# Optimization experiments

Measured on AMD Instinct MI355X. Metric: run time of the kernel, lower is better.

The kernel has to match this reference:

```python
import jax, jax.numpy as jnp
import numpy as np

K = 5
BASE_LAMBDA = 0.05
BASE_DELTA = 0.01
ITERS = 3
STEP = 0.2
FUSION_SCALE = 2.0
EPS = 1e-8


def _param_sets():
    # Deterministic (jitter_strength=0) version of SASConfig._generate_param_sets.
    # View 0 is identity; views 1..K-1 get linearly spaced lambda and coupled delta.
    lmin, lmax = BASE_LAMBDA * 0.5, BASE_LAMBDA * 1.5
    lams, deltas = [], []
    for i in range(K - 1):
        lam = lmin + (lmax - lmin) * i / max(1, K - 2)
        lams.append(lam)
        deltas.append(BASE_DELTA * np.sqrt(lam / (BASE_LAMBDA + 1e-8)))
    return jnp.asarray(lams, jnp.float32), jnp.asarray(deltas, jnp.float32)


def _huber_tv(x, lam, delta):
    # Anisotropic Huber-TV diffusion, skip_clamp=True (artifact denoising path).
    # x: [B,C,H,W]
    xd = x
    for _ in range(ITERS):
        dx = jnp.pad(xd[:, :, :, 1:] - xd[:, :, :, :-1], ((0, 0), (0, 0), (0, 0), (0, 1)))
        dy = jnp.pad(xd[:, :, 1:, :] - xd[:, :, :-1, :], ((0, 0), (0, 0), (0, 1), (0, 0)))
        gx = dx / (delta + jnp.abs(dx))
        gy = dy / (delta + jnp.abs(dy))
        # divergence with replicated first element (div[...,0] = g[...,0])
        div_x = gx - jnp.pad(gx[:, :, :, :-1], ((0, 0), (0, 0), (0, 0), (1, 0)))
        div_y = gy - jnp.pad(gy[:, :, :-1, :], ((0, 0), (0, 0), (1, 0), (0, 0)))
        xd = xd - STEP * (xd - x - lam * (div_x + div_y))
    return xd


def setup_inputs() -> dict:
    key = jax.random.key(0)
    x = jax.random.normal(key, (32, 3, 256, 256), dtype=jnp.float32)
    return {"x": x}


def reference(x):
    B = x.shape[0]
    # torch.median over flattened |artifact| (lower median for even count)
    flat = jnp.abs(x).reshape(B, -1)
    n = flat.shape[1]
    scale = jnp.sort(flat, axis=1)[:, (n - 1) // 2].reshape(B, 1, 1, 1) + 1e-8

    lams, deltas = _param_sets()
    xn = x / scale
    denoised = jax.vmap(lambda l, d: _huber_tv(xn, l, d))(lams, deltas)  # [K-1,B,C,H,W]
    arts = jnp.concatenate([x[None], denoised * scale[None]], axis=0)  # [K,B,C,H,W]

    # Robust MAD-weighted fusion (K=5 is odd, jnp.median == torch.median over dim 0)
    med = jnp.median(arts, axis=0)
    dev = jnp.abs(arts - med[None])
    mad = jnp.median(dev, axis=0)
    mad = jnp.maximum(mad, 0.1 * mad.mean())
    w = jnp.exp(-dev / (FUSION_SCALE * mad[None]))
    fused = (w * arts).sum(axis=0) / (w.sum(axis=0) + EPS)
    return fused
```

## Files before the change

### kernel.cpp

```cpp
#include <hip/hip_runtime.h>
#include <math.h>

typedef unsigned int u32;
typedef unsigned long long u64;

#define NPIX 6291456


__device__ __forceinline__ float med3f(float a, float b, float c) {
    return fmaxf(fminf(a, b), fminf(fmaxf(a, b), c));
}
__device__ __forceinline__ float med5f(float a0, float a1, float a2, float a3, float a4) {
    float mn01 = fminf(a0, a1), mx01 = fmaxf(a0, a1);
    float mn34 = fminf(a3, a4), mx34 = fmaxf(a3, a4);
    return med3f(a2, fmaxf(mn01, mn34), fminf(mx01, mx34));
}
__device__ __forceinline__ u32 packbf(float lo, float hi) {
    u32 a = __float_as_uint(lo), b = __float_as_uint(hi);
    a = (a + 0x7FFFu + ((a >> 16) & 1u)) >> 16;
    b = (b + 0x7FFFu + ((b >> 16) & 1u)) >> 16;
    return a | (b << 16);
}

__device__ __forceinline__ u32 scan1024(u32 v, u32* wtot) {
    int lane = threadIdx.x & 63, wid = threadIdx.x >> 6;
    u32 inc = v;
    #pragma unroll
    for (int off = 1; off < 64; off <<= 1) {
        u32 o = __shfl_up(inc, off);
        if (lane >= off) inc += o;
    }
    __syncthreads();
    if (lane == 63) wtot[wid] = inc;
    __syncthreads();
    for (int w = 0; w < wid; ++w) inc += wtot[w];
    return inc;
}


__global__ __launch_bounds__(1024) void hist_kernel(
        const float* __restrict__ x, u32* __restrict__ hist,
        float* __restrict__ madsum) {
    __shared__ u32 lh[16400];
    int b = blockIdx.x >> 3, s = blockIdx.x & 7, t = threadIdx.x;
    uint4 z = make_uint4(0u, 0u, 0u, 0u);
    #pragma unroll
    for (int j = 0; j < 4; ++j) ((uint4*)lh)[t + j * 1024] = z;
    if (t < 4) ((uint4*)lh)[4096 + t] = z;
    __syncthreads();
    const float4* xb = (const float4*)(x + (size_t)b * 196608 + s * 24576);
    u32 sub = (u32)(t & 3) * 4100u;
    #pragma unroll
    for (int i = 0; i < 6; ++i) {
        float4 v = xb[t + i * 1024];
        atomicAdd(&lh[sub + (__float_as_uint(fabsf(v.x)) >> 19)], 1u);
        atomicAdd(&lh[sub + (__float_as_uint(fabsf(v.y)) >> 19)], 1u);
        atomicAdd(&lh[sub + (__float_as_uint(fabsf(v.z)) >> 19)], 1u);
        atomicAdd(&lh[sub + (__float_as_uint(fabsf(v.w)) >> 19)], 1u);
    }
    __syncthreads();
    u32 a0 = 0, a1 = 0, a2 = 0, a3 = 0;
    #pragma unroll
    for (int sb = 0; sb < 4; ++sb) {
        uint4 hv = *(const uint4*)&lh[sb * 4100u + (u32)t * 4u];
        a0 += hv.x; a1 += hv.y; a2 += hv.z; a3 += hv.w;
    }
    u32* hb = hist + ((size_t)b * 8 + s) * 4096;
    ((uint4*)hb)[t] = make_uint4(a0, a1, a2, a3);
    if (s == 0 && t == 0 && b == 0) *madsum = 0.0f;
}


__global__ __launch_bounds__(1024) void extract_kernel(
        const float* __restrict__ x, const u32* __restrict__ hist,
        u32* __restrict__ members, u32* __restrict__ scount,
        u32* __restrict__ selBin, u32* __restrict__ selKr) {
    __shared__ u32 sbuf[8192];
    __shared__ u32 wtot[16];
    __shared__ u32 sBin, lcnt;
    int b = blockIdx.x >> 3, s = blockIdx.x & 7, t = threadIdx.x, lane = t & 63;
    if (t == 0) lcnt = 0u;
    const u32* hb = hist + (size_t)b * 32768;
    u32 s4[4] = {0u, 0u, 0u, 0u};
    #pragma unroll
    for (int sl = 0; sl < 8; ++sl) {
        uint4 h4 = ((const uint4*)(hb + sl * 4096))[t];
        s4[0] += h4.x; s4[1] += h4.y; s4[2] += h4.z; s4[3] += h4.w;
    }
    u32 sum = s4[0] + s4[1] + s4[2] + s4[3];
    u32 inc = scan1024(sum, wtot);
    u32 exc = inc - sum;
    u32 k = 98303u;
    if (exc <= k && k < inc) {
        u32 kr = k - exc;
        int j = 0;
        while (kr >= s4[j]) { kr -= s4[j]; ++j; }
        sBin = (u32)(t * 4 + j);
        if (s == 0) { selBin[b] = (u32)(t * 4 + j); selKr[b] = kr; }
    }
    __syncthreads();
    u32 bin = sBin;
    const float4* xb = (const float4*)(x + (size_t)b * 196608 + s * 24576);
    #pragma unroll 2
    for (int i = 0; i < 6; ++i) {
        float4 v = xb[t + i * 1024];
        float vv[4] = {v.x, v.y, v.z, v.w};
        #pragma unroll
        for (int e = 0; e < 4; ++e) {
            u32 bits = __float_as_uint(fabsf(vv[e]));
            bool is = (bits >> 19) == bin;
            u64 ball = __ballot(is);
            if (ball) {
                u32 cnt = (u32)__popcll(ball);
                u32 base = 0;
                if (lane == 0) base = atomicAdd(&lcnt, cnt);
                base = __shfl(base, 0);
                if (is) {
                    u32 p = base + (u32)__popcll(ball & ((1ull << lane) - 1ull));
                    if (p < 8192u) sbuf[p] = bits & 0x7FFFFu;
                }
            }
        }
    }
    __syncthreads();
    u32 cnt = lcnt; if (cnt > 8192u) cnt = 8192u;
    u32* mb = members + ((size_t)b * 8 + s) * 8192;
    for (u32 i = (u32)t; i < cnt; i += 1024u) mb[i] = sbuf[i];
    if (t == 0) scount[b * 8 + s] = cnt;
}


__global__ __launch_bounds__(1024) void select_kernel(
        const u32* __restrict__ scount, const u32* __restrict__ members,
        const u32* __restrict__ selBin, const u32* __restrict__ selKr,
        float* __restrict__ scale) {
    __shared__ u32 sbuf[8192];
    __shared__ u32 h[128];
    __shared__ u32 wtot[16];
    __shared__ u32 sPfx, sK;
    int b = blockIdx.x, t = threadIdx.x;
    u32 c[8], off[8], tot = 0u;
    #pragma unroll
    for (int s = 0; s < 8; ++s) {
        c[s] = scount[b * 8 + s];
        off[s] = tot;
        tot += c[s];
    }
    #pragma unroll
    for (int s = 0; s < 8; ++s) {
        const u32* mb = members + ((size_t)b * 8 + s) * 8192;
        for (u32 i = (u32)t; i < c[s]; i += 1024u) {
            u32 p = off[s] + i;
            if (p < 8192u) sbuf[p] = mb[i];
        }
    }
    u32 m = tot; if (m > 8192u) m = 8192u;
    if (t == 0) { sPfx = 0u; sK = selKr[b]; }
    __syncthreads();
    const int shf[3] = {12, 6, 0};
    const int wd[3]  = {7, 6, 6};
    const u32 msk[3] = {127u, 63u, 63u};
    #pragma unroll 1
    for (int rd = 0; rd < 3; ++rd) {
        u32 pfx = sPfx, k2 = sK;
        if (t < 128) h[t] = 0u;
        __syncthreads();
        for (u32 i = (u32)t; i < m; i += 1024u) {
            u32 v = sbuf[i];
            if ((v >> (shf[rd] + wd[rd])) == pfx)
                atomicAdd(&h[(v >> shf[rd]) & msk[rd]], 1u);
        }
        __syncthreads();
        u32 nb = msk[rd] + 1u;
        u32 cc = ((u32)t < nb) ? h[t] : 0u;
        u32 inc2 = scan1024(cc, wtot);
        u32 exc2 = inc2 - cc;
        if ((u32)t < nb && exc2 <= k2 && k2 < inc2) {
            sPfx = (pfx << wd[rd]) | (u32)t;
            sK = k2 - exc2;
        }
        __syncthreads();
    }
    if (t == 0)
        scale[b] = __uint_as_float((selBin[b] << 19) | sPfx) + 1e-8f;
}


__device__ __forceinline__ float dpp_shl1(float v) {
    return __uint_as_float((u32)__builtin_amdgcn_update_dpp(
        0, (int)__float_as_uint(v), 0x130, 0xF, 0xF, true));
}
__device__ __forceinline__ float dpp_shr1(float v) {
    return __uint_as_float((u32)__builtin_amdgcn_update_dpp(
        0, (int)__float_as_uint(v), 0x138, 0xF, 0xF, true));
}
__device__ __forceinline__ float hub(float d, float del) {
    return d * __builtin_amdgcn_rcpf(del + fabsf(d));
}
__device__ __forceinline__ float upd(float b, float xn, float dv, float lam) {
    float t = fmaf(-lam, dv, b - xn);
    return fmaf(-0.2f, t, b);
}

__device__ __forceinline__ float4 stage4(float4 B, float4 C, float4 xn, float4& gyp,
                                         int row, float mR3, float mL0,
                                         float lam, float del) {
    float mr = (row < 255) ? 1.f : 0.f;
    float m0 = (row == 0) ? 0.f : 1.f;
    float gy0 = hub(C.x - B.x, del) * mr;
    float gy1 = hub(C.y - B.y, del) * mr;
    float gy2 = hub(C.z - B.z, del) * mr;
    float gy3 = hub(C.w - B.w, del) * mr;
    float dv0 = gy0 - gyp.x * m0;
    float dv1 = gy1 - gyp.y * m0;
    float dv2 = gy2 - gyp.z * m0;
    float dv3 = gy3 - gyp.w * m0;
    gyp.x = gy0; gyp.y = gy1; gyp.z = gy2; gyp.w = gy3;
    float B0n = dpp_shl1(B.x);
    float g01 = hub(B.y - B.x, del);
    float g12 = hub(B.z - B.y, del);
    float g23 = hub(B.w - B.z, del);
    float g3n = hub(B0n - B.w, del) * mR3;
    float gp  = dpp_shr1(g3n) * mL0;
    float4 o;
    o.x = upd(B.x, xn.x, (g01 - gp)  + dv0, lam);
    o.y = upd(B.y, xn.y, (g12 - g01) + dv1, lam);
    o.z = upd(B.z, xn.z, (g23 - g12) + dv2, lam);
    o.w = upd(B.w, xn.w, (g3n - g23) + dv3, lam);
    return o;
}

__global__ __launch_bounds__(256, 6) void denoise_kernel(
        const float* __restrict__ x, const float* __restrict__ scale,
        u32* __restrict__ arts, float* __restrict__ madsum,
        float4 lam4, float4 del4) {
    __shared__ float sex[2][5][256];
    __shared__ float red[4];
    int t = threadIdx.x, lane = t & 63, wid = t >> 6;
    int img = blockIdx.x >> 3;
    int seg = blockIdx.x & 7;
    float sc = scale[img / 3];
    float lam = ((wid == 0) ? lam4.x : (wid == 1) ? lam4.y : (wid == 2) ? lam4.z : lam4.w) * sc;
    float del = ((wid == 0) ? del4.x : (wid == 1) ? del4.y : (wid == 2) ? del4.z : del4.w) * sc;
    float mR3 = (lane == 63) ? 0.f : 1.f;
    float mL0 = (lane == 0) ? 0.f : 1.f;
    const float4* xp = (const float4*)(x + (size_t)img * 65536) + lane;
    u32* ap = arts + (size_t)wid * (NPIX / 2) + (size_t)img * 32768 + lane * 2;

    float4 z4 = {0.f, 0.f, 0.f, 0.f};
    float4 cur1 = z4, cur2 = z4, gyp1 = z4, gyp2 = z4, gyp3 = z4;
    float4 n0 = z4, n1 = z4, n2 = z4;
    int out_lo = seg * 32, out_hi = out_lo + 31;
    int rs = (out_lo >= 3) ? out_lo - 3 : 0;
    int rend = out_hi + 3;
    float msum = 0.f;

    float4 nl = xp[rs << 6];
    for (int r = rs; r <= rend; ++r) {
        int rn = (r + 1 <= 255) ? r + 1 : 255;
        float4 nxt = xp[rn << 6];
        int r1 = r - 1, r2 = r - 2, r3 = r - 3;
        float4 x1 = stage4(n0,   nl, n0, gyp1, r1, mR3, mL0, lam, del);
        float4 x2 = stage4(cur1, x1, n1, gyp2, r2, mR3, mL0, lam, del);
        float4 x3 = stage4(cur2, x2, n2, gyp3, r3, mR3, mL0, lam, del);
        cur1 = x1; cur2 = x2;
        if (r3 >= out_lo) {
            uint2 pk;
            pk.x = packbf(x3.x, x3.y);
            pk.y = packbf(x3.z, x3.w);
            *(uint2*)(ap + (r3 << 7)) = pk;
            int pb = r3 & 1;
            *(float4*)&sex[pb][wid + 1][lane * 4] = x3;
            if (wid == 0) *(float4*)&sex[pb][0][lane * 4] = n2;
            __syncthreads();
            int c = wid * 64 + lane;
            float a0 = sex[pb][0][c], a1 = sex[pb][1][c], a2 = sex[pb][2][c],
                  a3 = sex[pb][3][c], a4 = sex[pb][4][c];
            float med = med5f(a0, a1, a2, a3, a4);
            msum += med5f(fabsf(a0 - med), fabsf(a1 - med), fabsf(a2 - med),
                          fabsf(a3 - med), fabsf(a4 - med));
        }
        n2 = n1; n1 = n0; n0 = nl;
        nl = nxt;
    }
    #pragma unroll
    for (int off = 32; off > 0; off >>= 1) msum += __shfl_down(msum, off);
    if (lane == 0) red[wid] = msum;
    __syncthreads();
    if (t == 0) atomicAdd(madsum, red[0] + red[1] + red[2] + red[3]);
}


__global__ __launch_bounds__(256) void fuse_kernel(
        const float* __restrict__ x, const u32* __restrict__ artsU,
        const float* __restrict__ madsum, float* __restrict__ out) {
    int t = blockIdx.x * 256 + threadIdx.x;
    float floorv = 0.1f * (*madsum) * (1.0f / 6291456.0f);
    float4 xv = ((const float4*)x)[t];
    uint2 q0 = ((const uint2*)(artsU))[t];
    uint2 q1 = ((const uint2*)(artsU + NPIX / 2))[t];
    uint2 q2 = ((const uint2*)(artsU + NPIX))[t];
    uint2 q3 = ((const uint2*)(artsU + 3 * (NPIX / 2)))[t];
    float4 o;
#define FUSE1(res, A0, U0, U1, U2, U3, SH) { \
        float a0 = A0; \
        float a1 = __uint_as_float(SH(U0)), a2 = __uint_as_float(SH(U1)); \
        float a3 = __uint_as_float(SH(U2)), a4 = __uint_as_float(SH(U3)); \
        float med = med5f(a0, a1, a2, a3, a4); \
        float d0 = fabsf(a0 - med), d1 = fabsf(a1 - med), d2 = fabsf(a2 - med); \
        float d3 = fabsf(a3 - med), d4 = fabsf(a4 - med); \
        float mad = med5f(d0, d1, d2, d3, d4); \
        float mm = fmaxf(mad, floorv); \
        float inv = 0.5f / mm; \
        float w0 = __expf(-d0 * inv), w1 = __expf(-d1 * inv), w2 = __expf(-d2 * inv); \
        float w3 = __expf(-d3 * inv), w4 = __expf(-d4 * inv); \
        float swt = w0 + w1 + w2 + w3 + w4; \
        float sva = fmaf(w0, a0, fmaf(w1, a1, fmaf(w2, a2, fmaf(w3, a3, w4 * a4)))); \
        res = sva / (swt + 1e-8f); \
    }
#define LO16(u) ((u) << 16)
#define HI16(u) ((u) & 0xFFFF0000u)
    FUSE1(o.x, xv.x, q0.x, q1.x, q2.x, q3.x, LO16);
    FUSE1(o.y, xv.y, q0.x, q1.x, q2.x, q3.x, HI16);
    FUSE1(o.z, xv.z, q0.y, q1.y, q2.y, q3.y, LO16);
    FUSE1(o.w, xv.w, q0.y, q1.y, q2.y, q3.y, HI16);
#undef FUSE1
#undef LO16
#undef HI16
    ((float4*)out)[t] = o;
}


extern "C" void kernel_launch(void* const* d_in, const int* in_sizes, int n_in,
                              void* d_out, int out_size, void* d_ws, size_t ws_size,
                              hipStream_t stream) {
    const float* x = (const float*)d_in[0];
    float* out = (float*)d_out;
    char* ws = (char*)d_ws;
    float* scale  = (float*)ws;
    float* madsum = (float*)(ws + 128);
    u32* selBin   = (u32*)(ws + 384);
    u32* selKr    = (u32*)(ws + 512);
    u32* artsU    = (u32*)(ws + 1024);
    u32* hist     = artsU;
    u32* members  = artsU + (size_t)32 * 8 * 4096;
    u32* scount   = members + (size_t)32 * 8 * 8192;

    hist_kernel<<<256, 1024, 0, stream>>>(x, hist, madsum);
    extract_kernel<<<256, 1024, 0, stream>>>(x, hist, members, scount, selBin, selKr);
    select_kernel<<<32, 1024, 0, stream>>>(scount, members, selBin, selKr, scale);

    float lamf[4], delf[4];
    for (int i = 0; i < 4; ++i) {
        double lam = 0.025 + 0.05 * (double)i / 3.0;
        lamf[i] = (float)lam;
        delf[i] = (float)(0.01 * sqrt(lam / (0.05 + 1e-8)));
    }
    float4 lam4 = make_float4(lamf[0], lamf[1], lamf[2], lamf[3]);
    float4 del4 = make_float4(delf[0], delf[1], delf[2], delf[3]);

    denoise_kernel<<<768, 256, 0, stream>>>(x, scale, artsU, madsum, lam4, del4);
    fuse_kernel<<<6144, 256, 0, stream>>>(x, artsU, madsum, out);
}
```

Before: 177.8 us.

## Merge all stages into one cooperative persistent kernel with grid syncs

```diff
diff --git a/kernel.cpp b/kernel.cpp
--- a/kernel.cpp
+++ b/kernel.cpp
@@ -1,10 +1,15 @@
 #include <hip/hip_runtime.h>
+#include <hip/hip_cooperative_groups.h>
 #include <math.h>
+
+namespace cg = cooperative_groups;
 
 typedef unsigned int u32;
 typedef unsigned long long u64;
 
 #define NPIX 6291456
+#define NBLK 768
+#define NTHR 256
 
 
 __device__ __forceinline__ float med3f(float a, float b, float c) {
@@ -22,7 +27,7 @@
     return a | (b << 16);
 }
 
-__device__ __forceinline__ u32 scan1024(u32 v, u32* wtot) {
+__device__ __forceinline__ u32 scan256(u32 v, u32* wtot) {
     int lane = threadIdx.x & 63, wid = threadIdx.x >> 6;
     u32 inc = v;
     #pragma unroll
@@ -38,72 +43,85 @@
 }
 
 
-__global__ __launch_bounds__(1024) void hist_kernel(
-        const float* __restrict__ x, u32* __restrict__ hist,
-        float* __restrict__ madsum) {
-    __shared__ u32 lh[16400];
-    int b = blockIdx.x >> 3, s = blockIdx.x & 7, t = threadIdx.x;
+__device__ void phase_hist(const float* __restrict__ x, u32* ghist,
+                           float* madsum, u32* shraw) {
+    int blk = blockIdx.x, t = threadIdx.x;
+    int b = blk / 24, s = blk % 24;
+    u32* lh = shraw;
     uint4 z = make_uint4(0u, 0u, 0u, 0u);
     #pragma unroll
-    for (int j = 0; j < 4; ++j) ((uint4*)lh)[t + j * 1024] = z;
-    if (t < 4) ((uint4*)lh)[4096 + t] = z;
-    __syncthreads();
-    const float4* xb = (const float4*)(x + (size_t)b * 196608 + s * 24576);
-    u32 sub = (u32)(t & 3) * 4100u;
-    #pragma unroll
-    for (int i = 0; i < 6; ++i) {
-        float4 v = xb[t + i * 1024];
-        atomicAdd(&lh[sub + (__float_as_uint(fabsf(v.x)) >> 19)], 1u);
-        atomicAdd(&lh[sub + (__float_as_uint(fabsf(v.y)) >> 19)], 1u);
-        atomicAdd(&lh[sub + (__float_as_uint(fabsf(v.z)) >> 19)], 1u);
-        atomicAdd(&lh[sub + (__float_as_uint(fabsf(v.w)) >> 19)], 1u);
-    }
-    __syncthreads();
-    u32 a0 = 0, a1 = 0, a2 = 0, a3 = 0;
-    #pragma unroll
-    for (int sb = 0; sb < 4; ++sb) {
-        uint4 hv = *(const uint4*)&lh[sb * 4100u + (u32)t * 4u];
-        a0 += hv.x; a1 += hv.y; a2 += hv.z; a3 += hv.w;
-    }
-    u32* hb = hist + ((size_t)b * 8 + s) * 4096;
-    ((uint4*)hb)[t] = make_uint4(a0, a1, a2, a3);
-    if (s == 0 && t == 0 && b == 0) *madsum = 0.0f;
-}
-
-
-__global__ __launch_bounds__(1024) void extract_kernel(
-        const float* __restrict__ x, const u32* __restrict__ hist,
-        u32* __restrict__ members, u32* __restrict__ scount,
-        u32* __restrict__ selBin, u32* __restrict__ selKr) {
-    __shared__ u32 sbuf[8192];
-    __shared__ u32 wtot[16];
-    __shared__ u32 sBin, lcnt;
-    int b = blockIdx.x >> 3, s = blockIdx.x & 7, t = threadIdx.x, lane = t & 63;
-    if (t == 0) lcnt = 0u;
-    const u32* hb = hist + (size_t)b * 32768;
-    u32 s4[4] = {0u, 0u, 0u, 0u};
-    #pragma unroll
-    for (int sl = 0; sl < 8; ++sl) {
-        uint4 h4 = ((const uint4*)(hb + sl * 4096))[t];
-        s4[0] += h4.x; s4[1] += h4.y; s4[2] += h4.z; s4[3] += h4.w;
-    }
-    u32 sum = s4[0] + s4[1] + s4[2] + s4[3];
-    u32 inc = scan1024(sum, wtot);
+    for (int j = 0; j < 4; ++j) ((uint4*)lh)[t + j * 256] = z;
+    __syncthreads();
+    const float4* xb = (const float4*)(x + (size_t)b * 196608 + s * 8192);
+    #pragma unroll
+    for (int i = 0; i < 8; ++i) {
+        float4 v = xb[t + i * 256];
+        atomicAdd(&lh[__float_as_uint(fabsf(v.x)) >> 19], 1u);
+        atomicAdd(&lh[__float_as_uint(fabsf(v.y)) >> 19], 1u);
+        atomicAdd(&lh[__float_as_uint(fabsf(v.z)) >> 19], 1u);
+        atomicAdd(&lh[__float_as_uint(fabsf(v.w)) >> 19], 1u);
+    }
+    __syncthreads();
+    uint4* ghb = (uint4*)(ghist + (size_t)blk * 4096);
+    #pragma unroll
+    for (int j = 0; j < 4; ++j) ghb[t + j * 256] = ((uint4*)lh)[t + j * 256];
+    if (blk == 0 && t == 0) *madsum = 0.0f;
+}
+
+
+__device__ void phase_binsel(const u32* ghist, u32* selBin, u32* selKr,
+                             u32* shraw) {
+    int blk = blockIdx.x;
+    if (blk >= 32) return;
+    int t = threadIdx.x;
+    u32* wtot = shraw;
+    u32 s16[16];
+    #pragma unroll
+    for (int j = 0; j < 16; ++j) s16[j] = 0u;
+    const u32* hb = ghist + (size_t)blk * 24 * 4096;
+    for (int sl = 0; sl < 24; ++sl) {
+        const uint4* hp = (const uint4*)(hb + sl * 4096);
+        #pragma unroll
+        for (int j = 0; j < 4; ++j) {
+            uint4 h4 = hp[t * 4 + j];
+            s16[4 * j + 0] += h4.x; s16[4 * j + 1] += h4.y;
+            s16[4 * j + 2] += h4.z; s16[4 * j + 3] += h4.w;
+        }
+    }
+    u32 sum = 0;
+    #pragma unroll
+    for (int j = 0; j < 16; ++j) sum += s16[j];
+    u32 inc = scan256(sum, wtot);
     u32 exc = inc - sum;
     u32 k = 98303u;
     if (exc <= k && k < inc) {
-        u32 kr = k - exc;
-        int j = 0;
-        while (kr >= s4[j]) { kr -= s4[j]; ++j; }
-        sBin = (u32)(t * 4 + j);
-        if (s == 0) { selBin[b] = (u32)(t * 4 + j); selKr[b] = kr; }
-    }
-    __syncthreads();
-    u32 bin = sBin;
-    const float4* xb = (const float4*)(x + (size_t)b * 196608 + s * 24576);
+        u32 kr = k - exc, acc = 0u;
+        #pragma unroll
+        for (int j = 0; j < 16; ++j) {
+            u32 nacc = acc + s16[j];
+            if (kr >= acc && kr < nacc) {
+                selBin[blk] = (u32)(t * 16 + j);
+                selKr[blk] = kr - acc;
+            }
+            acc = nacc;
+        }
+    }
+}
+
+
+__device__ void phase_extract(const float* __restrict__ x, const u32* selBin,
+                              u32* members, u32* scount, u32* shraw) {
+    int blk = blockIdx.x, t = threadIdx.x, lane = t & 63;
+    int b = blk / 24, s = blk % 24;
+    u32* sbuf = shraw;
+    u32* lcnt = shraw + 8192;
+    if (t == 0) *lcnt = 0u;
+    u32 bin = selBin[b];
+    __syncthreads();
+    const float4* xb = (const float4*)(x + (size_t)b * 196608 + s * 8192);
     #pragma unroll 2
-    for (int i = 0; i < 6; ++i) {
-        float4 v = xb[t + i * 1024];
+    for (int i = 0; i < 8; ++i) {
+        float4 v = xb[t + i * 256];
         float vv[4] = {v.x, v.y, v.z, v.w};
         #pragma unroll
         for (int e = 0; e < 4; ++e) {
@@ -113,7 +131,7 @@
             if (ball) {
                 u32 cnt = (u32)__popcll(ball);
                 u32 base = 0;
-                if (lane == 0) base = atomicAdd(&lcnt, cnt);
+                if (lane == 0) base = atomicAdd(lcnt, cnt);
                 base = __shfl(base, 0);
                 if (is) {
                     u32 p = base + (u32)__popcll(ball & ((1ull << lane) - 1ull));
@@ -123,49 +141,52 @@
         }
     }
     __syncthreads();
-    u32 cnt = lcnt; if (cnt > 8192u) cnt = 8192u;
-    u32* mb = members + ((size_t)b * 8 + s) * 8192;
-    for (u32 i = (u32)t; i < cnt; i += 1024u) mb[i] = sbuf[i];
-    if (t == 0) scount[b * 8 + s] = cnt;
-}
-
-
-__global__ __launch_bounds__(1024) void select_kernel(
-        const u32* __restrict__ scount, const u32* __restrict__ members,
-        const u32* __restrict__ selBin, const u32* __restrict__ selKr,
-        float* __restrict__ scale) {
-    __shared__ u32 sbuf[8192];
-    __shared__ u32 h[128];
-    __shared__ u32 wtot[16];
-    __shared__ u32 sPfx, sK;
-    int b = blockIdx.x, t = threadIdx.x;
-    u32 c[8], off[8], tot = 0u;
-    #pragma unroll
-    for (int s = 0; s < 8; ++s) {
-        c[s] = scount[b * 8 + s];
-        off[s] = tot;
-        tot += c[s];
-    }
-    #pragma unroll
-    for (int s = 0; s < 8; ++s) {
-        const u32* mb = members + ((size_t)b * 8 + s) * 8192;
-        for (u32 i = (u32)t; i < c[s]; i += 1024u) {
-            u32 p = off[s] + i;
+    u32 cnt = *lcnt; if (cnt > 8192u) cnt = 8192u;
+    u32* mb = members + (size_t)blk * 8192;
+    for (u32 i = (u32)t; i < cnt; i += 256u) mb[i] = sbuf[i];
+    if (t == 0) scount[blk] = cnt;
+}
+
+
+__device__ void phase_select(const u32* scount, const u32* members,
+                             const u32* selBin, const u32* selKr,
+                             float* scale, u32* shraw) {
+    int blk = blockIdx.x;
+    if (blk >= 32) return;
+    int t = threadIdx.x;
+    u32* sbuf = shraw;
+    u32* h    = shraw + 8192;
+    u32* wtot = shraw + 8320;
+    u32* soff = shraw + 8336;
+    u32* sPfx = shraw + 8364;
+    u32* sK   = shraw + 8365;
+    if (t == 0) {
+        u32 acc = 0u;
+        for (int sl = 0; sl < 24; ++sl) { soff[sl] = acc; acc += scount[blk * 24 + sl]; }
+        soff[24] = acc;
+        *sPfx = 0u;
+        *sK = selKr[blk];
+    }
+    __syncthreads();
+    for (int sl = 0; sl < 24; ++sl) {
+        u32 off = soff[sl], c = soff[sl + 1] - off;
+        const u32* mb = members + (size_t)(blk * 24 + sl) * 8192;
+        for (u32 i = (u32)t; i < c; i += 256u) {
+            u32 p = off + i;
             if (p < 8192u) sbuf[p] = mb[i];
         }
     }
-    u32 m = tot; if (m > 8192u) m = 8192u;
-    if (t == 0) { sPfx = 0u; sK = selKr[b]; }
+    u32 m = soff[24]; if (m > 8192u) m = 8192u;
     __syncthreads();
     const int shf[3] = {12, 6, 0};
     const int wd[3]  = {7, 6, 6};
     const u32 msk[3] = {127u, 63u, 63u};
     #pragma unroll 1
     for (int rd = 0; rd < 3; ++rd) {
-        u32 pfx = sPfx, k2 = sK;
+        u32 pfx = *sPfx, k2 = *sK;
         if (t < 128) h[t] = 0u;
         __syncthreads();
-        for (u32 i = (u32)t; i < m; i += 1024u) {
+        for (u32 i = (u32)t; i < m; i += 256u) {
             u32 v = sbuf[i];
             if ((v >> (shf[rd] + wd[rd])) == pfx)
                 atomicAdd(&h[(v >> shf[rd]) & msk[rd]], 1u);
@@ -173,16 +194,16 @@
         __syncthreads();
         u32 nb = msk[rd] + 1u;
         u32 cc = ((u32)t < nb) ? h[t] : 0u;
-        u32 inc2 = scan1024(cc, wtot);
+        u32 inc2 = scan256(cc, wtot);
         u32 exc2 = inc2 - cc;
         if ((u32)t < nb && exc2 <= k2 && k2 < inc2) {
-            sPfx = (pfx << wd[rd]) | (u32)t;
-            sK = k2 - exc2;
+            *sPfx = (pfx << wd[rd]) | (u32)t;
+            *sK = k2 - exc2;
         }
         __syncthreads();
     }
     if (t == 0)
-        scale[b] = __uint_as_float((selBin[b] << 19) | sPfx) + 1e-8f;
+        scale[blk] = __uint_as_float((selBin[blk] << 19) | *sPfx) + 1e-8f;
 }
 
 
@@ -230,12 +251,11 @@
     return o;
 }
 
-__global__ __launch_bounds__(256, 6) void denoise_kernel(
-        const float* __restrict__ x, const float* __restrict__ scale,
-        u32* __restrict__ arts, float* __restrict__ madsum,
-        float4 lam4, float4 del4) {
-    __shared__ float sex[2][5][256];
-    __shared__ float red[4];
+__device__ void phase_denoise(const float* __restrict__ x, const float* scale,
+                              u32* arts, float* madsum,
+                              float4 lam4, float4 del4, u32* shraw) {
+    float* sexf = (float*)shraw;
+    float* red  = sexf + 2560;
     int t = threadIdx.x, lane = t & 63, wid = t >> 6;
     int img = blockIdx.x >> 3;
     int seg = blockIdx.x & 7;
@@ -270,12 +290,13 @@
             pk.y = packbf(x3.z, x3.w);
             *(uint2*)(ap + (r3 << 7)) = pk;
             int pb = r3 & 1;
-            *(float4*)&sex[pb][wid + 1][lane * 4] = x3;
-            if (wid == 0) *(float4*)&sex[pb][0][lane * 4] = n2;
+            *(float4*)&sexf[pb * 1280 + (wid + 1) * 256 + lane * 4] = x3;
+            if (wid == 0) *(float4*)&sexf[pb * 1280 + lane * 4] = n2;
             __syncthreads();
             int c = wid * 64 + lane;
-            float a0 = sex[pb][0][c], a1 = sex[pb][1][c], a2 = sex[pb][2][c],
-                  a3 = sex[pb][3][c], a4 = sex[pb][4][c];
+            float a0 = sexf[pb * 1280 + c],       a1 = sexf[pb * 1280 + 256 + c];
+            float a2 = sexf[pb * 1280 + 512 + c], a3 = sexf[pb * 1280 + 768 + c];
+            float a4 = sexf[pb * 1280 + 1024 + c];
             float med = med5f(a0, a1, a2, a3, a4);
             msum += med5f(fabsf(a0 - med), fabsf(a1 - med), fabsf(a2 - med),
                           fabsf(a3 - med), fabsf(a4 - med));
@@ -291,17 +312,16 @@
 }
 
 
-__global__ __launch_bounds__(256) void fuse_kernel(
-        const float* __restrict__ x, const u32* __restrict__ artsU,
-        const float* __restrict__ madsum, float* __restrict__ out) {
-    int t = blockIdx.x * 256 + threadIdx.x;
+__device__ void phase_fuse(const float* __restrict__ x, const u32* artsU,
+                           const float* madsum, float* __restrict__ out) {
     float floorv = 0.1f * (*madsum) * (1.0f / 6291456.0f);
-    float4 xv = ((const float4*)x)[t];
-    uint2 q0 = ((const uint2*)(artsU))[t];
-    uint2 q1 = ((const uint2*)(artsU + NPIX / 2))[t];
-    uint2 q2 = ((const uint2*)(artsU + NPIX))[t];
-    uint2 q3 = ((const uint2*)(artsU + 3 * (NPIX / 2)))[t];
-    float4 o;
+    for (u32 t = blockIdx.x * 256u + threadIdx.x; t < NPIX / 4; t += NBLK * NTHR) {
+        float4 xv = ((const float4*)x)[t];
+        uint2 q0 = ((const uint2*)(artsU))[t];
+        uint2 q1 = ((const uint2*)(artsU + NPIX / 2))[t];
+        uint2 q2 = ((const uint2*)(artsU + NPIX))[t];
+        uint2 q3 = ((const uint2*)(artsU + 3 * (NPIX / 2)))[t];
+        float4 o;
 #define FUSE1(res, A0, U0, U1, U2, U3, SH) { \
         float a0 = A0; \
         float a1 = __uint_as_float(SH(U0)), a2 = __uint_as_float(SH(U1)); \
@@ -320,14 +340,36 @@
     }
 #define LO16(u) ((u) << 16)
 #define HI16(u) ((u) & 0xFFFF0000u)
-    FUSE1(o.x, xv.x, q0.x, q1.x, q2.x, q3.x, LO16);
-    FUSE1(o.y, xv.y, q0.x, q1.x, q2.x, q3.x, HI16);
-    FUSE1(o.z, xv.z, q0.y, q1.y, q2.y, q3.y, LO16);
-    FUSE1(o.w, xv.w, q0.y, q1.y, q2.y, q3.y, HI16);
+        FUSE1(o.x, xv.x, q0.x, q1.x, q2.x, q3.x, LO16);
+        FUSE1(o.y, xv.y, q0.x, q1.x, q2.x, q3.x, HI16);
+        FUSE1(o.z, xv.z, q0.y, q1.y, q2.y, q3.y, LO16);
+        FUSE1(o.w, xv.w, q0.y, q1.y, q2.y, q3.y, HI16);
 #undef FUSE1
 #undef LO16
 #undef HI16
-    ((float4*)out)[t] = o;
+        ((float4*)out)[t] = o;
+    }
+}
+
+
+__global__ __launch_bounds__(256, 4) void mega_kernel(
+        const float* __restrict__ x, float* __restrict__ out,
+        float* scale, float* madsum, u32* selBin, u32* selKr,
+        u32* ghist, u32* members, u32* scount, u32* arts,
+        float4 lam4, float4 del4, int plo, int phi) {
+    __shared__ __align__(16) u32 shraw[8448];
+    cg::grid_group grid = cg::this_grid();
+    for (int p = plo; p <= phi; ++p) {
+        switch (p) {
+            case 0: phase_hist(x, ghist, madsum, shraw); break;
+            case 1: phase_binsel(ghist, selBin, selKr, shraw); break;
+            case 2: phase_extract(x, selBin, members, scount, shraw); break;
+            case 3: phase_select(scount, members, selBin, selKr, scale, shraw); break;
+            case 4: phase_denoise(x, scale, arts, madsum, lam4, del4, shraw); break;
+            case 5: phase_fuse(x, arts, madsum, out); break;
+        }
+        if (p < phi) grid.sync();
+    }
 }
 
 
@@ -342,13 +384,9 @@
     u32* selBin   = (u32*)(ws + 384);
     u32* selKr    = (u32*)(ws + 512);
     u32* artsU    = (u32*)(ws + 1024);
-    u32* hist     = artsU;
-    u32* members  = artsU + (size_t)32 * 8 * 4096;
-    u32* scount   = members + (size_t)32 * 8 * 8192;
-
-    hist_kernel<<<256, 1024, 0, stream>>>(x, hist, madsum);
-    extract_kernel<<<256, 1024, 0, stream>>>(x, hist, members, scount, selBin, selKr);
-    select_kernel<<<32, 1024, 0, stream>>>(scount, members, selBin, selKr, scale);
+    u32* ghist    = artsU;
+    u32* members  = artsU + (size_t)3145728;
+    u32* scount   = artsU + (size_t)9437184;
 
     float lamf[4], delf[4];
     for (int i = 0; i < 4; ++i) {
@@ -359,6 +397,17 @@
     float4 lam4 = make_float4(lamf[0], lamf[1], lamf[2], lamf[3]);
     float4 del4 = make_float4(delf[0], delf[1], delf[2], delf[3]);
 
-    denoise_kernel<<<768, 256, 0, stream>>>(x, scale, artsU, madsum, lam4, del4);
-    fuse_kernel<<<6144, 256, 0, stream>>>(x, artsU, madsum, out);
-}
+    int plo = 0, phi = 5;
+    void* kargs[] = {(void*)&x, (void*)&out, (void*)&scale, (void*)&madsum,
+                     (void*)&selBin, (void*)&selKr, (void*)&ghist, (void*)&members,
+                     (void*)&scount, (void*)&artsU, (void*)&lam4, (void*)&del4,
+                     (void*)&plo, (void*)&phi};
+    hipError_t e = hipLaunchCooperativeKernel((void*)mega_kernel,
+                       dim3(NBLK), dim3(NTHR), kargs, 0, stream);
+    if (e != hipSuccess) {
+        (void)hipGetLastError();
+        for (int p = 0; p < 6; ++p)
+            mega_kernel<<<NBLK, NTHR, 0, stream>>>(x, out, scale, madsum,
+                selBin, selKr, ghist, members, scount, artsU, lam4, del4, p, p);
+    }
+}
```

Result: slower. 636.0 us (+257.7%).

## Merge stages with last-block reductions and a cooperative grid barrier

Applied to the files above, without the earlier changes.

```diff
diff --git a/kernel.cpp b/kernel.cpp
--- a/kernel.cpp
+++ b/kernel.cpp
@@ -5,6 +5,7 @@
 typedef unsigned long long u64;
 
 #define NPIX 6291456
+#define DBLK 768
 
 
 __device__ __forceinline__ float med3f(float a, float b, float c) {
@@ -39,9 +40,12 @@
 
 
 __global__ __launch_bounds__(1024) void hist_kernel(
-        const float* __restrict__ x, u32* __restrict__ hist,
-        float* __restrict__ madsum) {
+        const float* __restrict__ x, u32* __restrict__ ghist,
+        u32* __restrict__ arrive, u32* __restrict__ selBin,
+        u32* __restrict__ selKr) {
     __shared__ u32 lh[16400];
+    __shared__ u32 wtot[16];
+    __shared__ u32 sLast;
     int b = blockIdx.x >> 3, s = blockIdx.x & 7, t = threadIdx.x;
     uint4 z = make_uint4(0u, 0u, 0u, 0u);
     #pragma unroll
@@ -65,41 +69,52 @@
         uint4 hv = *(const uint4*)&lh[sb * 4100u + (u32)t * 4u];
         a0 += hv.x; a1 += hv.y; a2 += hv.z; a3 += hv.w;
     }
-    u32* hb = hist + ((size_t)b * 8 + s) * 4096;
+    u32* hb = ghist + ((size_t)b * 8 + s) * 4096;
     ((uint4*)hb)[t] = make_uint4(a0, a1, a2, a3);
-    if (s == 0 && t == 0 && b == 0) *madsum = 0.0f;
-}
-
-
-__global__ __launch_bounds__(1024) void extract_kernel(
-        const float* __restrict__ x, const u32* __restrict__ hist,
-        u32* __restrict__ members, u32* __restrict__ scount,
-        u32* __restrict__ selBin, u32* __restrict__ selKr) {
+    __threadfence();
+    __syncthreads();
+    if (t == 0) {
+        u32 old = atomicAdd(&arrive[b * 32], 1u);
+        sLast = (old == 7u) ? 1u : 0u;
+    }
+    __syncthreads();
+    if (sLast) {
+        __threadfence();
+        const u32* hball = ghist + (size_t)b * 32768;
+        u32 s4[4] = {0u, 0u, 0u, 0u};
+        #pragma unroll
+        for (int sl = 0; sl < 8; ++sl) {
+            uint4 h4 = ((const uint4*)(hball + sl * 4096))[t];
+            s4[0] += h4.x; s4[1] += h4.y; s4[2] += h4.z; s4[3] += h4.w;
+        }
+        u32 sum = s4[0] + s4[1] + s4[2] + s4[3];
+        u32 inc = scan1024(sum, wtot);
+        u32 exc = inc - sum;
+        u32 k = 98303u;
+        if (exc <= k && k < inc) {
+            u32 kr = k - exc;
+            int j = 0;
+            while (kr >= s4[j]) { kr -= s4[j]; ++j; }
+            selBin[b] = (u32)(t * 4 + j);
+            selKr[b] = kr;
+        }
+    }
+}
+
+
+__global__ __launch_bounds__(1024) void extsel_kernel(
+        const float* __restrict__ x, const u32* __restrict__ selBin,
+        const u32* __restrict__ selKr, u32* __restrict__ members,
+        u32* __restrict__ scount, u32* __restrict__ arrive,
+        float* __restrict__ scale) {
     __shared__ u32 sbuf[8192];
+    __shared__ u32 h[128];
     __shared__ u32 wtot[16];
-    __shared__ u32 sBin, lcnt;
+    __shared__ u32 lcnt, sLast, sPfx, sK;
     int b = blockIdx.x >> 3, s = blockIdx.x & 7, t = threadIdx.x, lane = t & 63;
     if (t == 0) lcnt = 0u;
-    const u32* hb = hist + (size_t)b * 32768;
-    u32 s4[4] = {0u, 0u, 0u, 0u};
-    #pragma unroll
-    for (int sl = 0; sl < 8; ++sl) {
-        uint4 h4 = ((const uint4*)(hb + sl * 4096))[t];
-        s4[0] += h4.x; s4[1] += h4.y; s4[2] += h4.z; s4[3] += h4.w;
-    }
-    u32 sum = s4[0] + s4[1] + s4[2] + s4[3];
-    u32 inc = scan1024(sum, wtot);
-    u32 exc = inc - sum;
-    u32 k = 98303u;
-    if (exc <= k && k < inc) {
-        u32 kr = k - exc;
-        int j = 0;
-        while (kr >= s4[j]) { kr -= s4[j]; ++j; }
-        sBin = (u32)(t * 4 + j);
-        if (s == 0) { selBin[b] = (u32)(t * 4 + j); selKr[b] = kr; }
-    }
-    __syncthreads();
-    u32 bin = sBin;
+    u32 bin = selBin[b];
+    __syncthreads();
     const float4* xb = (const float4*)(x + (size_t)b * 196608 + s * 24576);
     #pragma unroll 2
     for (int i = 0; i < 6; ++i) {
@@ -127,62 +142,60 @@
     u32* mb = members + ((size_t)b * 8 + s) * 8192;
     for (u32 i = (u32)t; i < cnt; i += 1024u) mb[i] = sbuf[i];
     if (t == 0) scount[b * 8 + s] = cnt;
-}
-
-
-__global__ __launch_bounds__(1024) void select_kernel(
-        const u32* __restrict__ scount, const u32* __restrict__ members,
-        const u32* __restrict__ selBin, const u32* __restrict__ selKr,
-        float* __restrict__ scale) {
-    __shared__ u32 sbuf[8192];
-    __shared__ u32 h[128];
-    __shared__ u32 wtot[16];
-    __shared__ u32 sPfx, sK;
-    int b = blockIdx.x, t = threadIdx.x;
-    u32 c[8], off[8], tot = 0u;
-    #pragma unroll
-    for (int s = 0; s < 8; ++s) {
-        c[s] = scount[b * 8 + s];
-        off[s] = tot;
-        tot += c[s];
-    }
-    #pragma unroll
-    for (int s = 0; s < 8; ++s) {
-        const u32* mb = members + ((size_t)b * 8 + s) * 8192;
-        for (u32 i = (u32)t; i < c[s]; i += 1024u) {
-            u32 p = off[s] + i;
-            if (p < 8192u) sbuf[p] = mb[i];
-        }
-    }
-    u32 m = tot; if (m > 8192u) m = 8192u;
-    if (t == 0) { sPfx = 0u; sK = selKr[b]; }
-    __syncthreads();
-    const int shf[3] = {12, 6, 0};
-    const int wd[3]  = {7, 6, 6};
-    const u32 msk[3] = {127u, 63u, 63u};
-    #pragma unroll 1
-    for (int rd = 0; rd < 3; ++rd) {
-        u32 pfx = sPfx, k2 = sK;
-        if (t < 128) h[t] = 0u;
+    __threadfence();
+    __syncthreads();
+    if (t == 0) {
+        u32 old = atomicAdd(&arrive[b * 32 + 16], 1u);
+        sLast = (old == 7u) ? 1u : 0u;
+    }
+    __syncthreads();
+    if (sLast) {
+        __threadfence();
+        u32 c8[8], off8[8], tot = 0u;
+        #pragma unroll
+        for (int sl = 0; sl < 8; ++sl) {
+            c8[sl] = scount[b * 8 + sl];
+            off8[sl] = tot;
+            tot += c8[sl];
+        }
+        #pragma unroll
+        for (int sl = 0; sl < 8; ++sl) {
+            const u32* mb2 = members + ((size_t)b * 8 + sl) * 8192;
+            for (u32 i = (u32)t; i < c8[sl]; i += 1024u) {
+                u32 p = off8[sl] + i;
+                if (p < 8192u) sbuf[p] = mb2[i];
+            }
+        }
+        u32 m = tot; if (m > 8192u) m = 8192u;
+        if (t == 0) { sPfx = 0u; sK = selKr[b]; }
         __syncthreads();
-        for (u32 i = (u32)t; i < m; i += 1024u) {
-            u32 v = sbuf[i];
-            if ((v >> (shf[rd] + wd[rd])) == pfx)
-                atomicAdd(&h[(v >> shf[rd]) & msk[rd]], 1u);
-        }
-        __syncthreads();
-        u32 nb = msk[rd] + 1u;
-        u32 cc = ((u32)t < nb) ? h[t] : 0u;
-        u32 inc2 = scan1024(cc, wtot);
-        u32 exc2 = inc2 - cc;
-        if ((u32)t < nb && exc2 <= k2 && k2 < inc2) {
-            sPfx = (pfx << wd[rd]) | (u32)t;
-            sK = k2 - exc2;
-        }
-        __syncthreads();
-    }
-    if (t == 0)
-        scale[b] = __uint_as_float((selBin[b] << 19) | sPfx) + 1e-8f;
+        const int shf[3] = {12, 6, 0};
+        const int wd[3]  = {7, 6, 6};
+        const u32 msk[3] = {127u, 63u, 63u};
+        #pragma unroll 1
+        for (int rd = 0; rd < 3; ++rd) {
+            u32 pfx = sPfx, k2 = sK;
+            if (t < 128) h[t] = 0u;
+            __syncthreads();
+            for (u32 i = (u32)t; i < m; i += 1024u) {
+                u32 v = sbuf[i];
+                if ((v >> (shf[rd] + wd[rd])) == pfx)
+                    atomicAdd(&h[(v >> shf[rd]) & msk[rd]], 1u);
+            }
+            __syncthreads();
+            u32 nb = msk[rd] + 1u;
+            u32 cc = ((u32)t < nb) ? h[t] : 0u;
+            u32 inc2 = scan1024(cc, wtot);
+            u32 exc2 = inc2 - cc;
+            if ((u32)t < nb && exc2 <= k2 && k2 < inc2) {
+                sPfx = (pfx << wd[rd]) | (u32)t;
+                sK = k2 - exc2;
+            }
+            __syncthreads();
+        }
+        if (t == 0)
+            scale[b] = __uint_as_float((selBin[b] << 19) | sPfx) + 1e-8f;
+    }
 }
 
 
@@ -230,77 +243,8 @@
     return o;
 }
 
-__global__ __launch_bounds__(256, 6) void denoise_kernel(
-        const float* __restrict__ x, const float* __restrict__ scale,
-        u32* __restrict__ arts, float* __restrict__ madsum,
-        float4 lam4, float4 del4) {
-    __shared__ float sex[2][5][256];
-    __shared__ float red[4];
-    int t = threadIdx.x, lane = t & 63, wid = t >> 6;
-    int img = blockIdx.x >> 3;
-    int seg = blockIdx.x & 7;
-    float sc = scale[img / 3];
-    float lam = ((wid == 0) ? lam4.x : (wid == 1) ? lam4.y : (wid == 2) ? lam4.z : lam4.w) * sc;
-    float del = ((wid == 0) ? del4.x : (wid == 1) ? del4.y : (wid == 2) ? del4.z : del4.w) * sc;
-    float mR3 = (lane == 63) ? 0.f : 1.f;
-    float mL0 = (lane == 0) ? 0.f : 1.f;
-    const float4* xp = (const float4*)(x + (size_t)img * 65536) + lane;
-    u32* ap = arts + (size_t)wid * (NPIX / 2) + (size_t)img * 32768 + lane * 2;
-
-    float4 z4 = {0.f, 0.f, 0.f, 0.f};
-    float4 cur1 = z4, cur2 = z4, gyp1 = z4, gyp2 = z4, gyp3 = z4;
-    float4 n0 = z4, n1 = z4, n2 = z4;
-    int out_lo = seg * 32, out_hi = out_lo + 31;
-    int rs = (out_lo >= 3) ? out_lo - 3 : 0;
-    int rend = out_hi + 3;
-    float msum = 0.f;
-
-    float4 nl = xp[rs << 6];
-    for (int r = rs; r <= rend; ++r) {
-        int rn = (r + 1 <= 255) ? r + 1 : 255;
-        float4 nxt = xp[rn << 6];
-        int r1 = r - 1, r2 = r - 2, r3 = r - 3;
-        float4 x1 = stage4(n0,   nl, n0, gyp1, r1, mR3, mL0, lam, del);
-        float4 x2 = stage4(cur1, x1, n1, gyp2, r2, mR3, mL0, lam, del);
-        float4 x3 = stage4(cur2, x2, n2, gyp3, r3, mR3, mL0, lam, del);
-        cur1 = x1; cur2 = x2;
-        if (r3 >= out_lo) {
-            uint2 pk;
-            pk.x = packbf(x3.x, x3.y);
-            pk.y = packbf(x3.z, x3.w);
-            *(uint2*)(ap + (r3 << 7)) = pk;
-            int pb = r3 & 1;
-            *(float4*)&sex[pb][wid + 1][lane * 4] = x3;
-            if (wid == 0) *(float4*)&sex[pb][0][lane * 4] = n2;
-            __syncthreads();
-            int c = wid * 64 + lane;
-            float a0 = sex[pb][0][c], a1 = sex[pb][1][c], a2 = sex[pb][2][c],
-                  a3 = sex[pb][3][c], a4 = sex[pb][4][c];
-            float med = med5f(a0, a1, a2, a3, a4);
-            msum += med5f(fabsf(a0 - med), fabsf(a1 - med), fabsf(a2 - med),
-                          fabsf(a3 - med), fabsf(a4 - med));
-        }
-        n2 = n1; n1 = n0; n0 = nl;
-        nl = nxt;
-    }
-    #pragma unroll
-    for (int off = 32; off > 0; off >>= 1) msum += __shfl_down(msum, off);
-    if (lane == 0) red[wid] = msum;
-    __syncthreads();
-    if (t == 0) atomicAdd(madsum, red[0] + red[1] + red[2] + red[3]);
-}
-
-
-__global__ __launch_bounds__(256) void fuse_kernel(
-        const float* __restrict__ x, const u32* __restrict__ artsU,
-        const float* __restrict__ madsum, float* __restrict__ out) {
-    int t = blockIdx.x * 256 + threadIdx.x;
-    float floorv = 0.1f * (*madsum) * (1.0f / 6291456.0f);
-    float4 xv = ((const float4*)x)[t];
-    uint2 q0 = ((const uint2*)(artsU))[t];
-    uint2 q1 = ((const uint2*)(artsU + NPIX / 2))[t];
-    uint2 q2 = ((const uint2*)(artsU + NPIX))[t];
-    uint2 q3 = ((const uint2*)(artsU + 3 * (NPIX / 2)))[t];
+__device__ __forceinline__ float4 fuse4(float4 xv, uint2 q0, uint2 q1,
+                                        uint2 q2, uint2 q3, float floorv) {
     float4 o;
 #define FUSE1(res, A0, U0, U1, U2, U3, SH) { \
         float a0 = A0; \
@@ -327,7 +271,110 @@
 #undef FUSE1
 #undef LO16
 #undef HI16
-    ((float4*)out)[t] = o;
+    return o;
+}
+
+__global__ __launch_bounds__(256, 6) void denofuse_kernel(
+        const float* __restrict__ x, const float* __restrict__ scale,
+        u32* __restrict__ arts, float* __restrict__ madsum,
+        u32* __restrict__ garrive, float* __restrict__ out,
+        float4 lam4, float4 del4, int doFuse) {
+    __shared__ float sexf[2 * 5 * 256 + 8];
+    float* red = sexf + 2560;
+    int t = threadIdx.x, lane = t & 63, wid = t >> 6;
+    int img = blockIdx.x >> 3;
+    int seg = blockIdx.x & 7;
+    float sc = scale[img / 3];
+    float lam = ((wid == 0) ? lam4.x : (wid == 1) ? lam4.y : (wid == 2) ? lam4.z : lam4.w) * sc;
+    float del = ((wid == 0) ? del4.x : (wid == 1) ? del4.y : (wid == 2) ? del4.z : del4.w) * sc;
+    float mR3 = (lane == 63) ? 0.f : 1.f;
+    float mL0 = (lane == 0) ? 0.f : 1.f;
+    const float4* xp = (const float4*)(x + (size_t)img * 65536) + lane;
+    u32* ap = arts + (size_t)wid * (NPIX / 2) + (size_t)img * 32768 + lane * 2;
+
+    float4 z4 = {0.f, 0.f, 0.f, 0.f};
+    float4 cur1 = z4, cur2 = z4, gyp1 = z4, gyp2 = z4, gyp3 = z4;
+    float4 n0 = z4, n1 = z4, n2 = z4;
+    int out_lo = seg * 32, out_hi = out_lo + 31;
+    int rs = (out_lo >= 3) ? out_lo - 3 : 0;
+    int rend = out_hi + 3;
+    float msum = 0.f;
+
+    float4 nl = xp[rs << 6];
+    for (int r = rs; r <= rend; ++r) {
+        int rn = (r + 1 <= 255) ? r + 1 : 255;
+        float4 nxt = xp[rn << 6];
+        int r1 = r - 1, r2 = r - 2, r3 = r - 3;
+        float4 x1 = stage4(n0,   nl, n0, gyp1, r1, mR3, mL0, lam, del);
+        float4 x2 = stage4(cur1, x1, n1, gyp2, r2, mR3, mL0, lam, del);
+        float4 x3 = stage4(cur2, x2, n2, gyp3, r3, mR3, mL0, lam, del);
+        cur1 = x1; cur2 = x2;
+        if (r3 >= out_lo) {
+            uint2 pk;
+            pk.x = packbf(x3.x, x3.y);
+            pk.y = packbf(x3.z, x3.w);
+            *(uint2*)(ap + (r3 << 7)) = pk;
+            int pb = r3 & 1;
+            *(float4*)&sexf[pb * 1280 + (wid + 1) * 256 + lane * 4] = x3;
+            if (wid == 0) *(float4*)&sexf[pb * 1280 + lane * 4] = n2;
+            __syncthreads();
+            int c = wid * 64 + lane;
+            float a0 = sexf[pb * 1280 + c],       a1 = sexf[pb * 1280 + 256 + c];
+            float a2 = sexf[pb * 1280 + 512 + c], a3 = sexf[pb * 1280 + 768 + c];
+            float a4 = sexf[pb * 1280 + 1024 + c];
+            float med = med5f(a0, a1, a2, a3, a4);
+            msum += med5f(fabsf(a0 - med), fabsf(a1 - med), fabsf(a2 - med),
+                          fabsf(a3 - med), fabsf(a4 - med));
+        }
+        n2 = n1; n1 = n0; n0 = nl;
+        nl = nxt;
+    }
+    #pragma unroll
+    for (int off = 32; off > 0; off >>= 1) msum += __shfl_down(msum, off);
+    if (lane == 0) red[wid] = msum;
+    __syncthreads();
+    if (t == 0) atomicAdd(madsum, red[0] + red[1] + red[2] + red[3]);
+    if (!doFuse) return;
+
+    if (t == 0) {
+        __threadfence();
+        atomicAdd(garrive, 1u);
+        while (__hip_atomic_load(garrive, __ATOMIC_ACQUIRE,
+                                 __HIP_MEMORY_SCOPE_AGENT) < (u32)DBLK)
+            __builtin_amdgcn_s_sleep(8);
+        __threadfence();
+        u32 mbits = __hip_atomic_load((u32*)madsum, __ATOMIC_ACQUIRE,
+                                      __HIP_MEMORY_SCOPE_AGENT);
+        sexf[2564] = __uint_as_float(mbits);
+    }
+    __syncthreads();
+    float floorv = 0.1f * sexf[2564] * (1.0f / 6291456.0f);
+
+    u32 base = (u32)img * 16384u + (u32)out_lo * 64u;
+    #pragma unroll 2
+    for (int i = 0; i < 8; ++i) {
+        u32 p = base + (u32)i * 256u + (u32)t;
+        float4 xv = ((const float4*)x)[p];
+        uint2 q0 = ((const uint2*)(arts))[p];
+        uint2 q1 = ((const uint2*)(arts + NPIX / 2))[p];
+        uint2 q2 = ((const uint2*)(arts + NPIX))[p];
+        uint2 q3 = ((const uint2*)(arts + 3 * (NPIX / 2)))[p];
+        ((float4*)out)[p] = fuse4(xv, q0, q1, q2, q3, floorv);
+    }
+}
+
+
+__global__ __launch_bounds__(256) void fuse_kernel(
+        const float* __restrict__ x, const u32* __restrict__ artsU,
+        const float* __restrict__ madsum, float* __restrict__ out) {
+    int t = blockIdx.x * 256 + threadIdx.x;
+    float floorv = 0.1f * (*madsum) * (1.0f / 6291456.0f);
+    float4 xv = ((const float4*)x)[t];
+    uint2 q0 = ((const uint2*)(artsU))[t];
+    uint2 q1 = ((const uint2*)(artsU + NPIX / 2))[t];
+    uint2 q2 = ((const uint2*)(artsU + NPIX))[t];
+    uint2 q3 = ((const uint2*)(artsU + 3 * (NPIX / 2)))[t];
+    ((float4*)out)[t] = fuse4(xv, q0, q1, q2, q3, floorv);
 }
 
 
@@ -338,17 +385,21 @@
     float* out = (float*)d_out;
     char* ws = (char*)d_ws;
     float* scale  = (float*)ws;
-    float* madsum = (float*)(ws + 128);
     u32* selBin   = (u32*)(ws + 384);
     u32* selKr    = (u32*)(ws + 512);
-    u32* artsU    = (u32*)(ws + 1024);
-    u32* hist     = artsU;
-    u32* members  = artsU + (size_t)32 * 8 * 4096;
-    u32* scount   = members + (size_t)32 * 8 * 8192;
-
-    hist_kernel<<<256, 1024, 0, stream>>>(x, hist, madsum);
-    extract_kernel<<<256, 1024, 0, stream>>>(x, hist, members, scount, selBin, selKr);
-    select_kernel<<<32, 1024, 0, stream>>>(scount, members, selBin, selKr, scale);
+    u32* arrive   = (u32*)(ws + 4096);
+    u32* garrive  = (u32*)(ws + 8192);
+    float* madsum = (float*)(ws + 8320);
+    u32* artsU    = (u32*)(ws + 12288);
+    u32* ghist    = artsU;
+    u32* members  = artsU + (size_t)1048576;
+    u32* scount   = artsU + (size_t)3145728;
+
+    hipMemsetAsync(ws + 4096, 0, 4352, stream);
+
+    hist_kernel<<<256, 1024, 0, stream>>>(x, ghist, arrive, selBin, selKr);
+    extsel_kernel<<<256, 1024, 0, stream>>>(x, selBin, selKr, members, scount,
+                                            arrive, scale);
 
     float lamf[4], delf[4];
     for (int i = 0; i < 4; ++i) {
@@ -359,6 +410,16 @@
     float4 lam4 = make_float4(lamf[0], lamf[1], lamf[2], lamf[3]);
     float4 del4 = make_float4(delf[0], delf[1], delf[2], delf[3]);
 
-    denoise_kernel<<<768, 256, 0, stream>>>(x, scale, artsU, madsum, lam4, del4);
-    fuse_kernel<<<6144, 256, 0, stream>>>(x, artsU, madsum, out);
-}
+    int doFuse = 1;
+    void* kargs[] = {(void*)&x, (void*)&scale, (void*)&artsU, (void*)&madsum,
+                     (void*)&garrive, (void*)&out, (void*)&lam4, (void*)&del4,
+                     (void*)&doFuse};
+    hipError_t e = hipLaunchCooperativeKernel((void*)denofuse_kernel,
+                       dim3(DBLK), dim3(256), kargs, 0, stream);
+    if (e != hipSuccess) {
+        (void)hipGetLastError();
+        denofuse_kernel<<<DBLK, 256, 0, stream>>>(x, scale, artsU, madsum,
+                                                  garrive, out, lam4, del4, 0);
+        fuse_kernel<<<12288, 256, 0, stream>>>(x, artsU, madsum, out);
+    }
+}
```

New measurement: 701.3 us. 3.94x slower.

## Fold median radix-select into denoise kernel and drop separate select launch

Applied to the files above, without the earlier changes.

```diff
diff --git a/kernel.cpp b/kernel.cpp
--- a/kernel.cpp
+++ b/kernel.cpp
@@ -23,6 +23,21 @@
 }
 
 __device__ __forceinline__ u32 scan1024(u32 v, u32* wtot) {
+    int lane = threadIdx.x & 63, wid = threadIdx.x >> 6;
+    u32 inc = v;
+    #pragma unroll
+    for (int off = 1; off < 64; off <<= 1) {
+        u32 o = __shfl_up(inc, off);
+        if (lane >= off) inc += o;
+    }
+    __syncthreads();
+    if (lane == 63) wtot[wid] = inc;
+    __syncthreads();
+    for (int w = 0; w < wid; ++w) inc += wtot[w];
+    return inc;
+}
+
+__device__ __forceinline__ u32 scan256(u32 v, u32* wtot) {
     int lane = threadIdx.x & 63, wid = threadIdx.x >> 6;
     u32 inc = v;
     #pragma unroll
@@ -127,62 +142,6 @@
     u32* mb = members + ((size_t)b * 8 + s) * 8192;
     for (u32 i = (u32)t; i < cnt; i += 1024u) mb[i] = sbuf[i];
     if (t == 0) scount[b * 8 + s] = cnt;
-}
-
-
-__global__ __launch_bounds__(1024) void select_kernel(
-        const u32* __restrict__ scount, const u32* __restrict__ members,
-        const u32* __restrict__ selBin, const u32* __restrict__ selKr,
-        float* __restrict__ scale) {
-    __shared__ u32 sbuf[8192];
-    __shared__ u32 h[128];
-    __shared__ u32 wtot[16];
-    __shared__ u32 sPfx, sK;
-    int b = blockIdx.x, t = threadIdx.x;
-    u32 c[8], off[8], tot = 0u;
-    #pragma unroll
-    for (int s = 0; s < 8; ++s) {
-        c[s] = scount[b * 8 + s];
-        off[s] = tot;
-        tot += c[s];
-    }
-    #pragma unroll
-    for (int s = 0; s < 8; ++s) {
-        const u32* mb = members + ((size_t)b * 8 + s) * 8192;
-        for (u32 i = (u32)t; i < c[s]; i += 1024u) {
-            u32 p = off[s] + i;
-            if (p < 8192u) sbuf[p] = mb[i];
-        }
-    }
-    u32 m = tot; if (m > 8192u) m = 8192u;
-    if (t == 0) { sPfx = 0u; sK = selKr[b]; }
-    __syncthreads();
-    const int shf[3] = {12, 6, 0};
-    const int wd[3]  = {7, 6, 6};
-    const u32 msk[3] = {127u, 63u, 63u};
-    #pragma unroll 1
-    for (int rd = 0; rd < 3; ++rd) {
-        u32 pfx = sPfx, k2 = sK;
-        if (t < 128) h[t] = 0u;
-        __syncthreads();
-        for (u32 i = (u32)t; i < m; i += 1024u) {
-            u32 v = sbuf[i];
-            if ((v >> (shf[rd] + wd[rd])) == pfx)
-                atomicAdd(&h[(v >> shf[rd]) & msk[rd]], 1u);
-        }
-        __syncthreads();
-        u32 nb = msk[rd] + 1u;
-        u32 cc = ((u32)t < nb) ? h[t] : 0u;
-        u32 inc2 = scan1024(cc, wtot);
-        u32 exc2 = inc2 - cc;
-        if ((u32)t < nb && exc2 <= k2 && k2 < inc2) {
-            sPfx = (pfx << wd[rd]) | (u32)t;
-            sK = k2 - exc2;
-        }
-        __syncthreads();
-    }
-    if (t == 0)
-        scale[b] = __uint_as_float((selBin[b] << 19) | sPfx) + 1e-8f;
 }
 
 
@@ -225,21 +184,71 @@
     float4 o;
     o.x = upd(B.x, xn.x, (g01 - gp)  + dv0, lam);
     o.y = upd(B.y, xn.y, (g12 - g01) + dv1, lam);
+    o.z = upd(B.z, xn.z, (g3n - g23) + dv3, lam);
+    o.w = 0.f;
     o.z = upd(B.z, xn.z, (g23 - g12) + dv2, lam);
     o.w = upd(B.w, xn.w, (g3n - g23) + dv3, lam);
     return o;
 }
 
 __global__ __launch_bounds__(256, 6) void denoise_kernel(
-        const float* __restrict__ x, const float* __restrict__ scale,
-        u32* __restrict__ arts, float* __restrict__ madsum,
-        float4 lam4, float4 del4) {
+        const float* __restrict__ x, const u32* __restrict__ selBin,
+        const u32* __restrict__ selKr, const u32* __restrict__ scount,
+        const u32* __restrict__ members, u32* __restrict__ arts,
+        float* __restrict__ madsum, float4 lam4, float4 del4) {
     __shared__ float sex[2][5][256];
     __shared__ float red[4];
+    __shared__ u32 h[128];
+    __shared__ u32 wt4[4];
+    __shared__ u32 sPfx, sK;
     int t = threadIdx.x, lane = t & 63, wid = t >> 6;
     int img = blockIdx.x >> 3;
     int seg = blockIdx.x & 7;
-    float sc = scale[img / 3];
+    int b = img / 3;
+
+    u32 bin = selBin[b];
+    u32 c8[8];
+    #pragma unroll
+    for (int sl = 0; sl < 8; ++sl) c8[sl] = scount[b * 8 + sl];
+    if (t == 0) { sPfx = 0u; sK = selKr[b]; }
+    __syncthreads();
+    {
+        const int shf[3] = {12, 6, 0};
+        const int wd[3]  = {7, 6, 6};
+        const u32 msk[3] = {127u, 63u, 63u};
+        #pragma unroll 1
+        for (int rd = 0; rd < 3; ++rd) {
+            u32 pfx = sPfx, k2 = sK;
+            if (t < 128) h[t] = 0u;
+            __syncthreads();
+            u32 off = 0u;
+            #pragma unroll
+            for (int sl = 0; sl < 8; ++sl) {
+                u32 lim = c8[sl];
+                if (off >= 8192u) lim = 0u;
+                else if (off + lim > 8192u) lim = 8192u - off;
+                const u32* mb = members + ((size_t)b * 8 + sl) * 8192;
+                for (u32 i = (u32)t; i < lim; i += 256u) {
+                    u32 v = mb[i];
+                    if ((v >> (shf[rd] + wd[rd])) == pfx)
+                        atomicAdd(&h[(v >> shf[rd]) & msk[rd]], 1u);
+                }
+                off += c8[sl];
+            }
+            __syncthreads();
+            u32 nb = msk[rd] + 1u;
+            u32 cc = ((u32)t < nb) ? h[t] : 0u;
+            u32 inc2 = scan256(cc, wt4);
+            u32 exc2 = inc2 - cc;
+            if ((u32)t < nb && exc2 <= k2 && k2 < inc2) {
+                sPfx = (pfx << wd[rd]) | (u32)t;
+                sK = k2 - exc2;
+            }
+            __syncthreads();
+        }
+    }
+    float sc = __uint_as_float((bin << 19) | sPfx) + 1e-8f;
+
     float lam = ((wid == 0) ? lam4.x : (wid == 1) ? lam4.y : (wid == 2) ? lam4.z : lam4.w) * sc;
     float del = ((wid == 0) ? del4.x : (wid == 1) ? del4.y : (wid == 2) ? del4.z : del4.w) * sc;
     float mR3 = (lane == 63) ? 0.f : 1.f;
@@ -337,18 +346,16 @@
     const float* x = (const float*)d_in[0];
     float* out = (float*)d_out;
     char* ws = (char*)d_ws;
-    float* scale  = (float*)ws;
-    float* madsum = (float*)(ws + 128);
+    float* madsum = (float*)ws;
     u32* selBin   = (u32*)(ws + 384);
     u32* selKr    = (u32*)(ws + 512);
     u32* artsU    = (u32*)(ws + 1024);
-    u32* hist     = artsU;
-    u32* members  = artsU + (size_t)32 * 8 * 4096;
+    u32* hist     = (u32*)out;
+    u32* members  = (u32*)out + (size_t)32 * 8 * 4096;
     u32* scount   = members + (size_t)32 * 8 * 8192;
 
     hist_kernel<<<256, 1024, 0, stream>>>(x, hist, madsum);
     extract_kernel<<<256, 1024, 0, stream>>>(x, hist, members, scount, selBin, selKr);
-    select_kernel<<<32, 1024, 0, stream>>>(scount, members, selBin, selKr, scale);
 
     float lamf[4], delf[4];
     for (int i = 0; i < 4; ++i) {
@@ -359,6 +366,7 @@
     float4 lam4 = make_float4(lamf[0], lamf[1], lamf[2], lamf[3]);
     float4 del4 = make_float4(delf[0], delf[1], delf[2], delf[3]);
 
-    denoise_kernel<<<768, 256, 0, stream>>>(x, scale, artsU, madsum, lam4, del4);
+    denoise_kernel<<<768, 256, 0, stream>>>(x, selBin, selKr, scount, members,
+                                            artsU, madsum, lam4, del4);
     fuse_kernel<<<6144, 256, 0, stream>>>(x, artsU, madsum, out);
 }
```

Measured after the change: 179.0 us. Within noise of the previous version (+0.7%).
